# Optimization experiments

Measured on AMD Instinct MI355X. Metric: run time of the kernel, lower is better.

The kernel has to match this reference:

```python
import jax, jax.numpy as jnp
import numpy as np

N_NODES = 50000
N_EDGES = 800000
N_GRAPHS = 64
D = 96              # input_dim = hidden_dim = output_dim
N_GIN = 4           # num_layers - 1 GINConv layers
N_HEADS = 5         # num_layers linear_prediction heads
BN_EPS = 1e-5


def setup_inputs() -> dict:
    key = jax.random.key(0)
    ks = jax.random.split(key, 16)
    s = 1.0 / np.sqrt(D)
    h = jax.random.normal(ks[0], (N_NODES, D), dtype=jnp.float32)
    src = jax.random.randint(ks[1], (N_EDGES,), 0, N_NODES, dtype=jnp.int32)
    dst = jax.random.randint(ks[2], (N_EDGES,), 0, N_NODES, dtype=jnp.int32)
    # sorted node->graph ids; deterministic so every graph is non-empty
    graph_ids = (jnp.arange(N_NODES, dtype=jnp.int32) * N_GRAPHS) // N_NODES
    return {
        "h": h,
        # GIN layer MLPs (num_mlp_layers=2): Linear -> BN -> ReLU -> Linear
        "gin_W1": jax.random.uniform(ks[3], (N_GIN, D, D), jnp.float32, -s, s),
        "gin_b1": jax.random.uniform(ks[4], (N_GIN, D), jnp.float32, -s, s),
        "gin_bn1_g": jnp.ones((N_GIN, D), jnp.float32),
        "gin_bn1_b": jnp.zeros((N_GIN, D), jnp.float32),
        "gin_W2": jax.random.uniform(ks[5], (N_GIN, D, D), jnp.float32, -s, s),
        "gin_b2": jax.random.uniform(ks[6], (N_GIN, D), jnp.float32, -s, s),
        # per-layer outer BatchNorm1d
        "bn_g": jnp.ones((N_GIN, D), jnp.float32),
        "bn_b": jnp.zeros((N_GIN, D), jnp.float32),
        # shared PReLU parameter (nn.PReLU default: 1 param, init 0.25)
        "prelu_a": jnp.full((1,), 0.25, jnp.float32),
        # linear_prediction heads
        "lin_W": jax.random.uniform(ks[7], (N_HEADS, D, D), jnp.float32, -s, s),
        "lin_b": jax.random.uniform(ks[8], (N_HEADS, D), jnp.float32, -s, s),
        "src": src,
        "dst": dst,
        "graph_ids": graph_ids,
    }


def _batchnorm(x, gamma, beta):
    # training-mode batch statistics over the node dim (biased variance, as torch)
    m = jnp.mean(x, axis=0)
    v = jnp.var(x, axis=0)
    return gamma * (x - m) * jax.lax.rsqrt(v + BN_EPS) + beta


def reference(h, gin_W1, gin_b1, gin_bn1_g, gin_bn1_b, gin_W2, gin_b2,
              bn_g, bn_b, prelu_a, lin_W, lin_b, src, dst, graph_ids):
    hidden_rep = [h]
    for l in range(N_GIN):
        # GINConv, sum aggregation, eps=0 (learn_eps=False): (1+eps)*h + sum_{j in N(i)} h_j
        agg = jax.ops.segment_sum(h[src], dst, num_segments=N_NODES)  # [N, D]
        z = h + agg
        # apply_func MLP: Linear -> BN -> ReLU -> Linear
        z = jax.nn.relu(_batchnorm(z @ gin_W1[l] + gin_b1[l], gin_bn1_g[l], gin_bn1_b[l]))
        z = z @ gin_W2[l] + gin_b2[l]
        # outer BatchNorm + PReLU
        z = _batchnorm(z, bn_g[l], bn_b[l])
        h = jnp.where(z >= 0, z, prelu_a * z)
        hidden_rep.append(h)
    # max graph pooling + per-layer linear heads (dropout = identity in eval)
    reps = []
    for l, hr in enumerate(hidden_rep):
        pooled = jax.ops.segment_max(hr, graph_ids, num_segments=N_GRAPHS)  # [B, D]
        reps.append(pooled @ lin_W[l] + lin_b[l])
    # layer_aggregation='cat': stack on dim=-1 then flatten -> [B, D * (N_GIN+1)]
    return jnp.stack(reps, axis=-1).reshape(N_GRAPHS, -1)
```

## Files before the change

kernel.cpp:

```cpp
#include <hip/hip_runtime.h>
#include <hip/hip_bf16.h>

#define N_NODES 50000
#define N_EDGES 800000
#define N_GRAPHS 64
#define D 96
#define N_GIN 4
#define BN_EPS 1e-5f
#define PCH 64
#define GEMM_GRID 782
#define LP 104
#define ELLCAP 64
#define SENT 50000

#define P1_BLOCKS 256
#define EPB 3125
#define BSH 8
#define BNODES 256
#define NBUCK 196
#define SPITCH 33

typedef __bf16 bf16;
typedef __bf16 bf16x8 __attribute__((ext_vector_type(8)));
typedef float f32x4 __attribute__((ext_vector_type(4)));
typedef unsigned short u16;
typedef unsigned int u32;
typedef unsigned short u16x8 __attribute__((ext_vector_type(8)));

__device__ inline unsigned enc(float f) {
    unsigned b = __float_as_uint(f);
    return (b & 0x80000000u) ? ~b : (b | 0x80000000u);
}
__device__ inline float dec(unsigned u) {
    return __uint_as_float((u & 0x80000000u) ? (u ^ 0x80000000u) : ~u);
}

__global__ void k_prolog(const float* __restrict__ h, bf16* __restrict__ hb,
                         bf16* __restrict__ hb1,
                         const float* __restrict__ W1, const float* __restrict__ W2,
                         bf16* __restrict__ wf, float* __restrict__ stats,
                         unsigned* __restrict__ pooledu) {
    int b = blockIdx.x;
    int tid = threadIdx.x;
    if (b < 2344) {
        int e = (b * 256 + tid) * 8;
        if (e >= N_NODES * D) return;
        float4 v0 = *(const float4*)(h + e);
        float4 v1 = *(const float4*)(h + e + 4);
        bf16x8 o;
        o[0] = (bf16)v0.x; o[1] = (bf16)v0.y; o[2] = (bf16)v0.z; o[3] = (bf16)v0.w;
        o[4] = (bf16)v1.x; o[5] = (bf16)v1.y; o[6] = (bf16)v1.z; o[7] = (bf16)v1.w;
        *(bf16x8*)(hb + e) = o;
    } else if (b < 2352) {
        int mat = b - 2344;
        const float* src = (mat < 4) ? (W1 + mat * D * D) : (W2 + (mat - 4) * D * D);
        bf16* dst = wf + mat * D * D;
        for (int p = tid; p < D * D; p += 256) {
            int f = p >> 9;
            int r = p & 511;
            int lane = r >> 3;
            int j = r & 7;
            int q = lane >> 4;
            int m16 = lane & 15;
            int nt = f / 3, ks = f % 3;
            int k = ks * 32 + q * 8 + j;
            int n = nt * 16 + m16;
            dst[p] = (bf16)src[k * D + n];
        }
    } else {
        int t = (b - 2352) * 256 + tid;
        if (t < N_GIN * 2 * 2 * D) stats[t] = 0.0f;
        if (t < 5 * N_GRAPHS * D) pooledu[t] = 0u;
        if (t < D) {
            hb[(size_t)SENT * D + t] = (bf16)0.0f;
            hb1[(size_t)SENT * D + t] = (bf16)0.0f;
        }
    }
}

__global__ void __launch_bounds__(256) k_part_pool(
        const int* __restrict__ src, const int* __restrict__ dst,
        u32* __restrict__ eo, u16* __restrict__ offs,
        const bf16* __restrict__ hb, unsigned* __restrict__ pooledu) {
    __shared__ u16 sdst[EPB + 3];
    __shared__ u16 ssrc[EPB + 3];
    __shared__ int hist[256];
    __shared__ int incl[256];
    int tid = threadIdx.x;
    if (blockIdx.x < P1_BLOCKS) {
        int e0 = blockIdx.x * EPB;
        hist[tid] = 0;
        __syncthreads();
        for (int i = tid; i < EPB; i += 256) {
            int d = dst[e0 + i];
            sdst[i] = (u16)d;
            ssrc[i] = (u16)src[e0 + i];
            atomicAdd(&hist[d >> BSH], 1);
        }
        __syncthreads();
        int v = hist[tid];
        incl[tid] = v;
        __syncthreads();
        for (int o = 1; o < 256; o <<= 1) {
            int t = (tid >= o) ? incl[tid - o] : 0;
            __syncthreads();
            incl[tid] += t;
            __syncthreads();
        }
        int ex = incl[tid] - v;
        if (tid <= NBUCK) offs[tid * P1_BLOCKS + blockIdx.x] = (u16)ex;
        hist[tid] = ex;
        __syncthreads();
        for (int i = tid; i < EPB; i += 256) {
            int d = sdst[i];
            int pos = atomicAdd(&hist[d >> BSH], 1);
            eo[e0 + pos] = ((u32)(d & (BNODES - 1)) << 16) | (u32)ssrc[i];
        }
    } else {
        int grp = (blockIdx.x - P1_BLOCKS) * 16 + (tid >> 4);
        int l = tid & 15;
        if (l >= 12) return;
        int g = grp / PCH, c = grp % PCH;
        int gs = (g * N_NODES + N_GRAPHS - 1) / N_GRAPHS;
        int ge = ((g + 1) * N_NODES + N_GRAPHS - 1) / N_GRAPHS;
        int len = ge - gs;
        int rs = gs + (len * c) / PCH;
        int re = gs + (len * (c + 1)) / PCH;
        const bf16x8* __restrict__ base = (const bf16x8*)hb;
        float m[8];
#pragma unroll
        for (int j = 0; j < 8; ++j) m[j] = -3e38f;
        int i = rs;
        for (; i + 2 <= re; i += 2) {
            bf16x8 r0 = base[i * 12 + l];
            bf16x8 r1 = base[(i + 1) * 12 + l];
#pragma unroll
            for (int j = 0; j < 8; ++j) m[j] = fmaxf(m[j], fmaxf((float)r0[j], (float)r1[j]));
        }
        if (i < re) {
            bf16x8 r = base[i * 12 + l];
#pragma unroll
            for (int j = 0; j < 8; ++j) m[j] = fmaxf(m[j], (float)r[j]);
        }
        unsigned* dstp = pooledu + (size_t)g * D + l * 8;
#pragma unroll
        for (int j = 0; j < 8; ++j) atomicMax(&dstp[j], enc(m[j]));
    }
}

__global__ void __launch_bounds__(256) k_ell_build(
        const u32* __restrict__ eo, const u16* __restrict__ offs,
        u16* __restrict__ ell, int* __restrict__ cnt) {
    __shared__ u32 sell32[BNODES * SPITCH];
    __shared__ int scnt[BNODES];
    int tid = threadIdx.x;
    int b = blockIdx.x;
    for (int i = tid; i < BNODES * SPITCH; i += 256) sell32[i] = 0xC350C350u;
    scnt[tid] = 0;
    __syncthreads();
    int beg = offs[b * P1_BLOCKS + tid];
    int end = offs[(b + 1) * P1_BLOCKS + tid];
    const u32* ep = eo + (size_t)tid * EPB;
    u16* srows = (u16*)sell32;
    for (int i = beg; i < end; ++i) {
        u32 pk = ep[i];
        int dl = pk >> 16;
        int pos = atomicAdd(&scnt[dl], 1);
        if (pos < ELLCAP) srows[dl * (2 * SPITCH) + pos] = (u16)pk;
    }
    __syncthreads();
    int node0 = b << BSH;
    int nn = min(BNODES, N_NODES - node0);
    if (tid < nn) cnt[node0 + tid] = scnt[tid];
    u32* gell = (u32*)(ell + (size_t)node0 * ELLCAP);
    for (int i = tid; i < nn * 32; i += 256) {
        gell[i] = sell32[(i >> 5) * SPITCH + (i & 31)];
    }
}

__global__ void __launch_bounds__(256) k_agg_gemm(
        const bf16* __restrict__ prev, const int* __restrict__ cnt,
        const u16* __restrict__ ell, const bf16* __restrict__ Bf,
        const float* __restrict__ bias, bf16* __restrict__ Z,
        float* __restrict__ ssum, float* __restrict__ sssq) {
    __shared__ bf16 sA[4][16 * LP];
    __shared__ float sr1[4][D], sr2[4][D];
    int tid = threadIdx.x;
    int lane = tid & 63, wv = tid >> 6;
    int q = lane >> 4, m16 = lane & 15;
    int strip = blockIdx.x * 4 + wv;

    float psum[6], pssq[6];
#pragma unroll
    for (int f = 0; f < 6; ++f) { psum[f] = 0.0f; pssq[f] = 0.0f; }

    if (strip < 3125) {
        const bf16x8* __restrict__ base = (const bf16x8*)prev;
        int gl = m16;
        if (gl < 12) {
#pragma unroll 1
            for (int rp = 0; rp < 2; ++rp) {
                int nA = strip * 16 + rp * 8 + q;
                int nB = nA + 4;
                float accA[8], accB[8];
                bf16x8 selfA = base[nA * 12 + gl];
                bf16x8 selfB = base[nB * 12 + gl];
#pragma unroll
                for (int j = 0; j < 8; ++j) { accA[j] = (float)selfA[j]; accB[j] = (float)selfB[j]; }
                int dgA = cnt[nA]; if (dgA > ELLCAP) dgA = ELLCAP;
                int dgB = cnt[nB]; if (dgB > ELLCAP) dgB = ELLCAP;
                int dgr = (((dgA > dgB) ? dgA : dgB) + 7) & ~7;
                const u16* epA = ell + (size_t)nA * ELLCAP;
                const u16* epB = ell + (size_t)nB * ELLCAP;
                u16x8 ivA = *(const u16x8*)(epA);
                u16x8 ivB = *(const u16x8*)(epB);
                for (int e = 0; e < dgr; e += 8) {
                    u16x8 nxA = *(const u16x8*)(epA + e + 8);
                    u16x8 nxB = *(const u16x8*)(epB + e + 8);
                    bf16x8 a0 = base[(int)ivA[0] * 12 + gl];
                    bf16x8 a1 = base[(int)ivA[1] * 12 + gl];
                    bf16x8 a2 = base[(int)ivA[2] * 12 + gl];
                    bf16x8 a3 = base[(int)ivA[3] * 12 + gl];
                    bf16x8 a4 = base[(int)ivA[4] * 12 + gl];
                    bf16x8 a5 = base[(int)ivA[5] * 12 + gl];
                    bf16x8 a6 = base[(int)ivA[6] * 12 + gl];
                    bf16x8 a7 = base[(int)ivA[7] * 12 + gl];
                    bf16x8 b0 = base[(int)ivB[0] * 12 + gl];
                    bf16x8 b1 = base[(int)ivB[1] * 12 + gl];
                    bf16x8 b2 = base[(int)ivB[2] * 12 + gl];
                    bf16x8 b3 = base[(int)ivB[3] * 12 + gl];
                    bf16x8 b4 = base[(int)ivB[4] * 12 + gl];
                    bf16x8 b5 = base[(int)ivB[5] * 12 + gl];
                    bf16x8 b6 = base[(int)ivB[6] * 12 + gl];
                    bf16x8 b7 = base[(int)ivB[7] * 12 + gl];
#pragma unroll
                    for (int j = 0; j < 8; ++j) {
                        accA[j] += (float)a0[j] + (float)a1[j] + (float)a2[j] + (float)a3[j]
                                 + (float)a4[j] + (float)a5[j] + (float)a6[j] + (float)a7[j];
                        accB[j] += (float)b0[j] + (float)b1[j] + (float)b2[j] + (float)b3[j]
                                 + (float)b4[j] + (float)b5[j] + (float)b6[j] + (float)b7[j];
                    }
                    ivA = nxA;
                    ivB = nxB;
                }
                bf16x8 oA, oB;
#pragma unroll
                for (int j = 0; j < 8; ++j) { oA[j] = (bf16)accA[j]; oB[j] = (bf16)accB[j]; }
                *(bf16x8*)&sA[wv][(rp * 8 + q) * LP + gl * 8] = oA;
                *(bf16x8*)&sA[wv][(rp * 8 + 4 + q) * LP + gl * 8] = oB;
            }
        }
        __asm__ volatile("s_waitcnt lgkmcnt(0)" ::: "memory");

        bf16x8 bfr[18];
#pragma unroll
        for (int f = 0; f < 18; ++f) bfr[f] = *(const bf16x8*)(Bf + (f * 64 + lane) * 8);

        bf16x8 a0 = *(const bf16x8*)&sA[wv][m16 * LP + q * 8];
        bf16x8 a1 = *(const bf16x8*)&sA[wv][m16 * LP + 32 + q * 8];
        bf16x8 a2 = *(const bf16x8*)&sA[wv][m16 * LP + 64 + q * 8];

#pragma unroll
        for (int f = 0; f < 6; ++f) {
            f32x4 acc = {0.0f, 0.0f, 0.0f, 0.0f};
            acc = __builtin_amdgcn_mfma_f32_16x16x32_bf16(a0, bfr[f * 3 + 0], acc, 0, 0, 0);
            acc = __builtin_amdgcn_mfma_f32_16x16x32_bf16(a1, bfr[f * 3 + 1], acc, 0, 0, 0);
            acc = __builtin_amdgcn_mfma_f32_16x16x32_bf16(a2, bfr[f * 3 + 2], acc, 0, 0, 0);
            int col = f * 16 + m16;
            float bvf = bias[col];
            bf16* zp = Z + (size_t)(strip * 16 + q * 4) * D + col;
#pragma unroll
            for (int i = 0; i < 4; ++i) {
                float v = acc[i] + bvf;
                zp[(size_t)i * D] = (bf16)v;
                psum[f] += v;
                pssq[f] += v * v;
            }
        }
    }
#pragma unroll
    for (int f = 0; f < 6; ++f) {
        float r = psum[f];
        r += __shfl_xor(r, 16);
        r += __shfl_xor(r, 32);
        float r2 = pssq[f];
        r2 += __shfl_xor(r2, 16);
        r2 += __shfl_xor(r2, 32);
        if (lane < 16) {
            sr1[wv][f * 16 + lane] = r;
            sr2[wv][f * 16 + lane] = r2;
        }
    }
    __syncthreads();
    int t = wv * 64 + lane;
    if (t < D) {
        atomicAdd(&ssum[t], sr1[0][t] + sr1[1][t] + sr1[2][t] + sr1[3][t]);
    } else if (t < 2 * D) {
        int u = t - D;
        atomicAdd(&sssq[u], sr2[0][u] + sr2[1][u] + sr2[2][u] + sr2[3][u]);
    }
}

__global__ void k_transform(const bf16* __restrict__ Z, const float* __restrict__ st,
                            const float* __restrict__ gamma, const float* __restrict__ beta,
                            const float* __restrict__ pa, bf16* __restrict__ O) {
    __shared__ float cs[D], ct[D];
    int t = threadIdx.x;
    if (t < D) {
        float m = st[t] * (1.0f / N_NODES);
        float v = st[D + t] * (1.0f / N_NODES) - m * m;
        float inv = rsqrtf(v + BN_EPS);
        float sc = gamma[t] * inv;
        cs[t] = sc;
        ct[t] = beta[t] - m * sc;
    }
    __syncthreads();
    int e = (blockIdx.x * 256 + t) * 8;
    if (e >= N_NODES * D) return;
    float alpha = pa[0];
    int c = e % D;
    bf16x8 z = *(const bf16x8*)(Z + e);
    bf16x8 o;
#pragma unroll
    for (int j = 0; j < 8; ++j) {
        float v = (float)z[j] * cs[c + j] + ct[c + j];
        o[j] = (bf16)(v >= 0.0f ? v : alpha * v);
    }
    *(bf16x8*)(O + e) = o;
}

__global__ void __launch_bounds__(256) k_gemm_fused(
        const bf16* __restrict__ A, const bf16* __restrict__ Bf,
        const float* __restrict__ st, const float* __restrict__ gamma,
        const float* __restrict__ beta, const float* __restrict__ bias,
        bf16* __restrict__ Z, float* __restrict__ ssum, float* __restrict__ sssq,
        unsigned* __restrict__ poolu) {
    __shared__ float cs[D], ct[D];
    __shared__ float sr1[4][D];
    __shared__ float sr2[4][D];
    __shared__ unsigned pmax[2 * D];
    int tid = threadIdx.x;
    if (tid < D) {
        float m = st[tid] * (1.0f / N_NODES);
        float v = st[D + tid] * (1.0f / N_NODES) - m * m;
        float inv = rsqrtf(v + BN_EPS);
        float sc = gamma[tid] * inv;
        cs[tid] = sc;
        ct[tid] = beta[tid] - m * sc;
    }
    if (tid < 2 * D) pmax[tid] = 0u;
    __syncthreads();

    int lane = tid & 63;
    int wv = tid >> 6;
    int w = (blockIdx.x * blockDim.x + tid) >> 6;
    int nw = (gridDim.x * blockDim.x) >> 6;
    int q = lane >> 4, m16 = lane & 15;
    int g0 = (int)(((long long)blockIdx.x * 64) * N_GRAPHS / N_NODES);

    float as_[3][8], at_[3][8];
#pragma unroll
    for (int ks = 0; ks < 3; ++ks)
#pragma unroll
        for (int j = 0; j < 8; ++j) {
            as_[ks][j] = cs[ks * 32 + q * 8 + j];
            at_[ks][j] = ct[ks * 32 + q * 8 + j];
        }

    bf16x8 bfr[18];
#pragma unroll
    for (int f = 0; f < 18; ++f) bfr[f] = *(const bf16x8*)(Bf + (f * 64 + lane) * 8);
    float bv[6];
#pragma unroll
    for (int f = 0; f < 6; ++f) bv[f] = bias[f * 16 + m16];
    float psum[6], pssq[6];
#pragma unroll
    for (int f = 0; f < 6; ++f) { psum[f] = 0.0f; pssq[f] = 0.0f; }

    const int NSTRIP = N_NODES / 16;
    for (int s = w; s < NSTRIP; s += nw) {
        const bf16* arow = A + (size_t)(s * 16 + m16) * D;
        bf16x8 z0 = *(const bf16x8*)(arow + q * 8);
        bf16x8 z1 = *(const bf16x8*)(arow + 32 + q * 8);
        bf16x8 z2 = *(const bf16x8*)(arow + 64 + q * 8);
        bf16x8 a0, a1, a2;
#pragma unroll
        for (int j = 0; j < 8; ++j) {
            a0[j] = (bf16)fmaxf(0.0f, (float)z0[j] * as_[0][j] + at_[0][j]);
            a1[j] = (bf16)fmaxf(0.0f, (float)z1[j] * as_[1][j] + at_[1][j]);
            a2[j] = (bf16)fmaxf(0.0f, (float)z2[j] * as_[2][j] + at_[2][j]);
        }
#pragma unroll
        for (int f = 0; f < 6; ++f) {
            f32x4 acc = {0.0f, 0.0f, 0.0f, 0.0f};
            acc = __builtin_amdgcn_mfma_f32_16x16x32_bf16(a0, bfr[f * 3 + 0], acc, 0, 0, 0);
            acc = __builtin_amdgcn_mfma_f32_16x16x32_bf16(a1, bfr[f * 3 + 1], acc, 0, 0, 0);
            acc = __builtin_amdgcn_mfma_f32_16x16x32_bf16(a2, bfr[f * 3 + 2], acc, 0, 0, 0);
            int col = f * 16 + m16;
            bf16* zp = Z + (size_t)(s * 16 + q * 4) * D + col;
#pragma unroll
            for (int i = 0; i < 4; ++i) {
                float v = acc[i] + bv[f];
                zp[(size_t)i * D] = (bf16)v;
                psum[f] += v;
                pssq[f] += v * v;
                int row = s * 16 + q * 4 + i;
                int g = (int)(((unsigned)row * 64u) / 50000u);
                int slot = g - g0;
                if (slot >= 0 && slot < 2)
                    atomicMax(&pmax[slot * D + col], enc(v));
            }
        }
    }
#pragma unroll
    for (int f = 0; f < 6; ++f) {
        float r = psum[f];
        r += __shfl_xor(r, 16);
        r += __shfl_xor(r, 32);
        float r2 = pssq[f];
        r2 += __shfl_xor(r2, 16);
        r2 += __shfl_xor(r2, 32);
        if (lane < 16) {
            sr1[wv][f * 16 + lane] = r;
            sr2[wv][f * 16 + lane] = r2;
        }
    }
    __syncthreads();
    int t = wv * 64 + lane;
    if (t < D) {
        atomicAdd(&ssum[t], sr1[0][t] + sr1[1][t] + sr1[2][t] + sr1[3][t]);
    } else if (t < 2 * D) {
        int u = t - D;
        atomicAdd(&sssq[u], sr2[0][u] + sr2[1][u] + sr2[2][u] + sr2[3][u]);
    }
    if (t < 2 * D) {
        int sl = t / D, c = t % D;
        int gg = g0 + sl;
        if (gg < N_GRAPHS && pmax[t] != 0u)
            atomicMax(&poolu[gg * D + c], pmax[t]);
    }
}

__global__ void k_heads(const unsigned* __restrict__ pooledu, const float* __restrict__ stats,
                        const float* __restrict__ bng, const float* __restrict__ bnb,
                        const float* __restrict__ pa, const float* __restrict__ W,
                        const float* __restrict__ B, float* __restrict__ out) {
    __shared__ float pv[D];
    int b = blockIdx.x;
    int l = b >> 6;
    int g = b & 63;
    int d = threadIdx.x;
    if (d < D) {
        float m = dec(pooledu[(size_t)(l * N_GRAPHS + g) * D + d]);
        if (l > 0) {
            int gl = l - 1;
            const float* st = stats + (gl * 2 + 1) * 2 * D;
            float mean = st[d] * (1.0f / N_NODES);
            float var = st[D + d] * (1.0f / N_NODES) - mean * mean;
            float inv = rsqrtf(var + BN_EPS);
            float s = bng[gl * D + d] * inv;
            float t = bnb[gl * D + d] - mean * s;
            float v = m * s + t;
            m = (v >= 0.0f) ? v : pa[0] * v;
        }
        pv[d] = m;
    }
    __syncthreads();
    if (d >= D) return;
    const float* w = W + (size_t)l * D * D;
    float acc = B[l * D + d];
    for (int k = 0; k < D; ++k) acc += pv[k] * w[k * D + d];
    out[g * (5 * D) + d * 5 + l] = acc;
}

extern "C" void kernel_launch(void* const* d_in, const int* in_sizes, int n_in,
                              void* d_out, int out_size, void* d_ws, size_t ws_size,
                              hipStream_t stream) {
    const float* h     = (const float*)d_in[0];
    const float* gW1   = (const float*)d_in[1];
    const float* gb1   = (const float*)d_in[2];
    const float* bn1g  = (const float*)d_in[3];
    const float* bn1b  = (const float*)d_in[4];
    const float* gW2   = (const float*)d_in[5];
    const float* gb2   = (const float*)d_in[6];
    const float* bng   = (const float*)d_in[7];
    const float* bnb   = (const float*)d_in[8];
    const float* prelu = (const float*)d_in[9];
    const float* linW  = (const float*)d_in[10];
    const float* linb  = (const float*)d_in[11];
    const int*   srcv  = (const int*)d_in[12];
    const int*   dstv  = (const int*)d_in[13];
    float* out = (float*)d_out;

    char* base = (char*)d_ws;
    size_t off = 0;
    auto carve = [&](size_t bytes) -> void* {
        void* p = base + off;
        off += (bytes + 255) & ~(size_t)255;
        return p;
    };
    const size_t HB = (size_t)N_NODES * D;
    bf16* hb0   = (bf16*)carve((HB + D) * 2);
    bf16* hb1   = (bf16*)carve((HB + D) * 2);
    bf16* zb    = (bf16*)carve(HB * 2);
    bf16* ab    = (bf16*)carve(HB * 2);
    bf16* wf    = (bf16*)carve(8 * D * D * 2);
    float* stats = (float*)carve(N_GIN * 2 * 2 * D * 4);
    int* cnt    = (int*)carve((size_t)N_NODES * 4);
    u16* ell    = (u16*)carve((size_t)N_NODES * ELLCAP * 2);
    u32* eo     = (u32*)carve((size_t)N_EDGES * 4);
    u16* offs   = (u16*)carve((size_t)(NBUCK + 1) * P1_BLOCKS * 2);
    unsigned* pooledu = (unsigned*)carve(5 * N_GRAPHS * D * 4);

    k_prolog<<<2472, 256, 0, stream>>>(h, hb0, hb1, gW1, gW2, wf, stats, pooledu);
    k_part_pool<<<P1_BLOCKS + N_GRAPHS * PCH / 16, 256, 0, stream>>>(
        srcv, dstv, eo, offs, hb0, pooledu);
    k_ell_build<<<NBUCK, 256, 0, stream>>>(eo, offs, ell, cnt);

    const bf16* prev = hb0;
    for (int l = 0; l < N_GIN; ++l) {
        float* st1 = stats + (l * 2 + 0) * 2 * D;
        float* st2 = stats + (l * 2 + 1) * 2 * D;
        if (l > 0) {
            float* stp = stats + ((l - 1) * 2 + 1) * 2 * D;
            k_transform<<<2344, 256, 0, stream>>>(ab, stp, bng + (l - 1) * D,
                                                  bnb + (l - 1) * D, prelu, hb1);
            prev = hb1;
        }
        k_agg_gemm<<<GEMM_GRID, 256, 0, stream>>>(prev, cnt, ell, wf + l * D * D,
                                                  gb1 + l * D, zb, st1, st1 + D);
        k_gemm_fused<<<GEMM_GRID, 256, 0, stream>>>(zb, wf + (4 + l) * D * D, st1,
                                                    bn1g + l * D, bn1b + l * D,
                                                    gb2 + l * D, ab, st2, st2 + D,
                                                    pooledu + (size_t)(l + 1) * N_GRAPHS * D);
    }
    k_heads<<<5 * N_GRAPHS, 128, 0, stream>>>(pooledu, stats, bng, bnb, prelu,
                                              linW, linb, out);
}
```

Baseline: 430.1 us.

## Split fused aggregation+GEMM into separate gather kernel and grid-stride GEMM kernel

Unfuses the neighbor-sum aggregation from the first MLP GEMM. The aggregation becomes its own kernel with more waves, each handling 8 nodes, and writes a bf16 buffer to global memory. A separate grid-stride GEMM kernel then reads that buffer and hoists the weight and bias loads out of the strip loop. The aim is more parallelism and occupancy for the latency-bound gather, at the cost of an extra global round trip of about 10 MB per layer and one extra launch per layer.

```diff
diff --git a/kernel.cpp b/kernel.cpp
--- a/kernel.cpp
+++ b/kernel.cpp
@@ -9,6 +9,7 @@
 #define BN_EPS 1e-5f
 #define PCH 64
 #define GEMM_GRID 782
+#define AGG_GRID 1563
 #define LP 104
 #define ELLCAP 64
 #define SENT 50000
@@ -178,88 +179,93 @@
     }
 }
 
-__global__ void __launch_bounds__(256) k_agg_gemm(
+__global__ void __launch_bounds__(256) k_agg(
         const bf16* __restrict__ prev, const int* __restrict__ cnt,
-        const u16* __restrict__ ell, const bf16* __restrict__ Bf,
+        const u16* __restrict__ ell, bf16* __restrict__ aggb) {
+    int tid = threadIdx.x;
+    int lane = tid & 63, wv = tid >> 6;
+    int q = lane >> 4, gl = lane & 15;
+    int w = blockIdx.x * 4 + wv;
+    if (w >= 6250 || gl >= 12) return;
+    const bf16x8* __restrict__ base = (const bf16x8*)prev;
+    int nA = w * 8 + q * 2;
+    int nB = nA + 1;
+    float accA[8], accB[8];
+    bf16x8 selfA = base[nA * 12 + gl];
+    bf16x8 selfB = base[nB * 12 + gl];
+#pragma unroll
+    for (int j = 0; j < 8; ++j) { accA[j] = (float)selfA[j]; accB[j] = (float)selfB[j]; }
+    int dgA = cnt[nA]; if (dgA > ELLCAP) dgA = ELLCAP;
+    int dgB = cnt[nB]; if (dgB > ELLCAP) dgB = ELLCAP;
+    int dgr = (((dgA > dgB) ? dgA : dgB) + 7) & ~7;
+    const u16* epA = ell + (size_t)nA * ELLCAP;
+    const u16* epB = ell + (size_t)nB * ELLCAP;
+    u16x8 ivA = *(const u16x8*)(epA);
+    u16x8 ivB = *(const u16x8*)(epB);
+    for (int e = 0; e < dgr; e += 8) {
+        u16x8 nxA = *(const u16x8*)(epA + e + 8);
+        u16x8 nxB = *(const u16x8*)(epB + e + 8);
+        bf16x8 a0 = base[(int)ivA[0] * 12 + gl];
+        bf16x8 a1 = base[(int)ivA[1] * 12 + gl];
+        bf16x8 a2 = base[(int)ivA[2] * 12 + gl];
+        bf16x8 a3 = base[(int)ivA[3] * 12 + gl];
+        bf16x8 a4 = base[(int)ivA[4] * 12 + gl];
+        bf16x8 a5 = base[(int)ivA[5] * 12 + gl];
+        bf16x8 a6 = base[(int)ivA[6] * 12 + gl];
+        bf16x8 a7 = base[(int)ivA[7] * 12 + gl];
+        bf16x8 b0 = base[(int)ivB[0] * 12 + gl];
+        bf16x8 b1 = base[(int)ivB[1] * 12 + gl];
+        bf16x8 b2 = base[(int)ivB[2] * 12 + gl];
+        bf16x8 b3 = base[(int)ivB[3] * 12 + gl];
+        bf16x8 b4 = base[(int)ivB[4] * 12 + gl];
+        bf16x8 b5 = base[(int)ivB[5] * 12 + gl];
+        bf16x8 b6 = base[(int)ivB[6] * 12 + gl];
+        bf16x8 b7 = base[(int)ivB[7] * 12 + gl];
+#pragma unroll
+        for (int j = 0; j < 8; ++j) {
+            accA[j] += (float)a0[j] + (float)a1[j] + (float)a2[j] + (float)a3[j]
+                     + (float)a4[j] + (float)a5[j] + (float)a6[j] + (float)a7[j];
+            accB[j] += (float)b0[j] + (float)b1[j] + (float)b2[j] + (float)b3[j]
+                     + (float)b4[j] + (float)b5[j] + (float)b6[j] + (float)b7[j];
+        }
+        ivA = nxA;
+        ivB = nxB;
+    }
+    bf16x8 oA, oB;
+#pragma unroll
+    for (int j = 0; j < 8; ++j) { oA[j] = (bf16)accA[j]; oB[j] = (bf16)accB[j]; }
+    *(bf16x8*)(aggb + (size_t)nA * D + gl * 8) = oA;
+    *(bf16x8*)(aggb + (size_t)nB * D + gl * 8) = oB;
+}
+
+__global__ void __launch_bounds__(256) k_gemm1(
+        const bf16* __restrict__ A, const bf16* __restrict__ Bf,
         const float* __restrict__ bias, bf16* __restrict__ Z,
         float* __restrict__ ssum, float* __restrict__ sssq) {
-    __shared__ bf16 sA[4][16 * LP];
     __shared__ float sr1[4][D], sr2[4][D];
     int tid = threadIdx.x;
-    int lane = tid & 63, wv = tid >> 6;
+    int lane = tid & 63;
+    int wv = tid >> 6;
+    int w = (blockIdx.x * blockDim.x + tid) >> 6;
+    int nw = (gridDim.x * blockDim.x) >> 6;
     int q = lane >> 4, m16 = lane & 15;
-    int strip = blockIdx.x * 4 + wv;
-
+
+    bf16x8 bfr[18];
+#pragma unroll
+    for (int f = 0; f < 18; ++f) bfr[f] = *(const bf16x8*)(Bf + (f * 64 + lane) * 8);
+    float bv[6];
+#pragma unroll
+    for (int f = 0; f < 6; ++f) bv[f] = bias[f * 16 + m16];
     float psum[6], pssq[6];
 #pragma unroll
     for (int f = 0; f < 6; ++f) { psum[f] = 0.0f; pssq[f] = 0.0f; }
 
-    if (strip < 3125) {
-        const bf16x8* __restrict__ base = (const bf16x8*)prev;
-        int gl = m16;
-        if (gl < 12) {
-#pragma unroll 1
-            for (int rp = 0; rp < 2; ++rp) {
-                int nA = strip * 16 + rp * 8 + q;
-                int nB = nA + 4;
-                float accA[8], accB[8];
-                bf16x8 selfA = base[nA * 12 + gl];
-                bf16x8 selfB = base[nB * 12 + gl];
-#pragma unroll
-                for (int j = 0; j < 8; ++j) { accA[j] = (float)selfA[j]; accB[j] = (float)selfB[j]; }
-                int dgA = cnt[nA]; if (dgA > ELLCAP) dgA = ELLCAP;
-                int dgB = cnt[nB]; if (dgB > ELLCAP) dgB = ELLCAP;
-                int dgr = (((dgA > dgB) ? dgA : dgB) + 7) & ~7;
-                const u16* epA = ell + (size_t)nA * ELLCAP;
-                const u16* epB = ell + (size_t)nB * ELLCAP;
-                u16x8 ivA = *(const u16x8*)(epA);
-                u16x8 ivB = *(const u16x8*)(epB);
-                for (int e = 0; e < dgr; e += 8) {
-                    u16x8 nxA = *(const u16x8*)(epA + e + 8);
-                    u16x8 nxB = *(const u16x8*)(epB + e + 8);
-                    bf16x8 a0 = base[(int)ivA[0] * 12 + gl];
-                    bf16x8 a1 = base[(int)ivA[1] * 12 + gl];
-                    bf16x8 a2 = base[(int)ivA[2] * 12 + gl];
-                    bf16x8 a3 = base[(int)ivA[3] * 12 + gl];
-                    bf16x8 a4 = base[(int)ivA[4] * 12 + gl];
-                    bf16x8 a5 = base[(int)ivA[5] * 12 + gl];
-                    bf16x8 a6 = base[(int)ivA[6] * 12 + gl];
-                    bf16x8 a7 = base[(int)ivA[7] * 12 + gl];
-                    bf16x8 b0 = base[(int)ivB[0] * 12 + gl];
-                    bf16x8 b1 = base[(int)ivB[1] * 12 + gl];
-                    bf16x8 b2 = base[(int)ivB[2] * 12 + gl];
-                    bf16x8 b3 = base[(int)ivB[3] * 12 + gl];
-                    bf16x8 b4 = base[(int)ivB[4] * 12 + gl];
-                    bf16x8 b5 = base[(int)ivB[5] * 12 + gl];
-                    bf16x8 b6 = base[(int)ivB[6] * 12 + gl];
-                    bf16x8 b7 = base[(int)ivB[7] * 12 + gl];
-#pragma unroll
-                    for (int j = 0; j < 8; ++j) {
-                        accA[j] += (float)a0[j] + (float)a1[j] + (float)a2[j] + (float)a3[j]
-                                 + (float)a4[j] + (float)a5[j] + (float)a6[j] + (float)a7[j];
-                        accB[j] += (float)b0[j] + (float)b1[j] + (float)b2[j] + (float)b3[j]
-                                 + (float)b4[j] + (float)b5[j] + (float)b6[j] + (float)b7[j];
-                    }
-                    ivA = nxA;
-                    ivB = nxB;
-                }
-                bf16x8 oA, oB;
-#pragma unroll
-                for (int j = 0; j < 8; ++j) { oA[j] = (bf16)accA[j]; oB[j] = (bf16)accB[j]; }
-                *(bf16x8*)&sA[wv][(rp * 8 + q) * LP + gl * 8] = oA;
-                *(bf16x8*)&sA[wv][(rp * 8 + 4 + q) * LP + gl * 8] = oB;
-            }
-        }
-        __asm__ volatile("s_waitcnt lgkmcnt(0)" ::: "memory");
-
-        bf16x8 bfr[18];
-#pragma unroll
-        for (int f = 0; f < 18; ++f) bfr[f] = *(const bf16x8*)(Bf + (f * 64 + lane) * 8);
-
-        bf16x8 a0 = *(const bf16x8*)&sA[wv][m16 * LP + q * 8];
-        bf16x8 a1 = *(const bf16x8*)&sA[wv][m16 * LP + 32 + q * 8];
-        bf16x8 a2 = *(const bf16x8*)&sA[wv][m16 * LP + 64 + q * 8];
-
+    const int NSTRIP = N_NODES / 16;
+    for (int s = w; s < NSTRIP; s += nw) {
+        const bf16* arow = A + (size_t)(s * 16 + m16) * D;
+        bf16x8 a0 = *(const bf16x8*)(arow + q * 8);
+        bf16x8 a1 = *(const bf16x8*)(arow + 32 + q * 8);
+        bf16x8 a2 = *(const bf16x8*)(arow + 64 + q * 8);
 #pragma unroll
         for (int f = 0; f < 6; ++f) {
             f32x4 acc = {0.0f, 0.0f, 0.0f, 0.0f};
@@ -267,11 +273,10 @@
             acc = __builtin_amdgcn_mfma_f32_16x16x32_bf16(a1, bfr[f * 3 + 1], acc, 0, 0, 0);
             acc = __builtin_amdgcn_mfma_f32_16x16x32_bf16(a2, bfr[f * 3 + 2], acc, 0, 0, 0);
             int col = f * 16 + m16;
-            float bvf = bias[col];
-            bf16* zp = Z + (size_t)(strip * 16 + q * 4) * D + col;
+            bf16* zp = Z + (size_t)(s * 16 + q * 4) * D + col;
 #pragma unroll
             for (int i = 0; i < 4; ++i) {
-                float v = acc[i] + bvf;
+                float v = acc[i] + bv[f];
                 zp[(size_t)i * D] = (bf16)v;
                 psum[f] += v;
                 pssq[f] += v * v;
@@ -502,6 +507,7 @@
     const size_t HB = (size_t)N_NODES * D;
     bf16* hb0   = (bf16*)carve((HB + D) * 2);
     bf16* hb1   = (bf16*)carve((HB + D) * 2);
+    bf16* aggb  = (bf16*)carve(HB * 2);
     bf16* zb    = (bf16*)carve(HB * 2);
     bf16* ab    = (bf16*)carve(HB * 2);
     bf16* wf    = (bf16*)carve(8 * D * D * 2);
@@ -527,8 +533,9 @@
                                                   bnb + (l - 1) * D, prelu, hb1);
             prev = hb1;
         }
-        k_agg_gemm<<<GEMM_GRID, 256, 0, stream>>>(prev, cnt, ell, wf + l * D * D,
-                                                  gb1 + l * D, zb, st1, st1 + D);
+        k_agg<<<AGG_GRID, 256, 0, stream>>>(prev, cnt, ell, aggb);
+        k_gemm1<<<GEMM_GRID, 256, 0, stream>>>(aggb, wf + l * D * D, gb1 + l * D,
+                                               zb, st1, st1 + D);
         k_gemm_fused<<<GEMM_GRID, 256, 0, stream>>>(zb, wf + (4 + l) * D * D, st1,
                                                     bn1g + l * D, bn1b + l * D,
                                                     gb2 + l * D, ab, st2, st2 + D,
```

New measurement: 460.4 us. 1.07x slower.
